# Kernel tuning notes

Hardware: AMD Instinct MI355X
Metric: run time of the kernel (lower is better)

The kernel has to match this reference:

```python
import jax, jax.numpy as jnp
import numpy as np

T, B, D, O = 2048, 32, 512, 512


def setup_inputs() -> dict:
    key = jax.random.key(0)
    ks = jax.random.split(key, 12)
    s = 0.02
    return {
        "word": jax.random.normal(ks[0], (T, B, D), dtype=jnp.float32),
        "Wf": jax.random.normal(ks[1], (D, D), dtype=jnp.float32) * s,
        "bf": jax.random.normal(ks[2], (D,), dtype=jnp.float32) * s,
        "Wi": jax.random.normal(ks[3], (D, D), dtype=jnp.float32) * s,
        "bi": jax.random.normal(ks[4], (D,), dtype=jnp.float32) * s,
        "Wz": jax.random.normal(ks[5], (D, D), dtype=jnp.float32) * s,
        "bz": jax.random.normal(ks[6], (D,), dtype=jnp.float32) * s,
        "Wo": jax.random.normal(ks[7], (D, D), dtype=jnp.float32) * s,
        "bo": jax.random.normal(ks[8], (D,), dtype=jnp.float32) * s,
        "Wy": jax.random.normal(ks[9], (O, D), dtype=jnp.float32) * s,
        "by": jax.random.normal(ks[10], (O,), dtype=jnp.float32) * s,
    }


def reference(word, Wf, bf, Wi, bi, Wz, bz, Wo, bo, Wy, by):
    # Faithful to the original buggy module:
    #  - forward discards the updated cell state, so c == 0 every step and
    #    the zf gate (wf) never affects the output.
    #  - z and zo reuse wi(hidden) instead of wz/wo(hidden).
    #  - the same Linear is applied to letter and hidden, so bias is doubled
    #    in zi (and zf).
    Bsz, Dd = word.shape[1], word.shape[2]

    def step(h, x):  # h: [B, D], x: [B, D]
        hWi = h @ Wi.T                                  # reused by zi, z, zo
        zi = jax.nn.sigmoid(x @ Wi.T + hWi + 2.0 * bi)
        z = jax.nn.sigmoid(x @ Wz.T + bz + hWi + bi)
        zo = jax.nn.sigmoid(x @ Wo.T + bo + hWi + bi)
        c = zi * z                                      # zf * 0 + zi * z
        h_new = zo * jnp.tanh(c)
        return h_new, None

    h0 = jnp.zeros((Bsz, Dd), dtype=word.dtype)
    h_final, _ = jax.lax.scan(step, h0, word)
    # original computes wy(hidden) every step but only returns the last one
    output = h_final @ Wy.T + by                        # [B, O]
    return output
```

## Files before the change

kernel.cpp:

```cpp
#include <hip/hip_runtime.h>

typedef unsigned int u32;
typedef unsigned short u16;
typedef _Float16 f16;
typedef f16 f16x2 __attribute__((ext_vector_type(2)));

__device__ __forceinline__ float fdot2(u32 a, u32 b, float c) {
#if __has_builtin(__builtin_amdgcn_fdot2)
    return __builtin_amdgcn_fdot2(__builtin_bit_cast(f16x2, a),
                                  __builtin_bit_cast(f16x2, b), c, false);
#else
    f16x2 av = __builtin_bit_cast(f16x2, a), bv = __builtin_bit_cast(f16x2, b);
    c += (float)av[0] * (float)bv[0];
    c += (float)av[1] * (float)bv[1];
    return c;
#endif
}

__device__ __forceinline__ u32 pack2h(float a, float b) {
    f16x2 h; h[0] = (f16)a; h[1] = (f16)b;
    return __builtin_bit_cast(u32, h);
}
__device__ __forceinline__ float h2f(u16 x) { return (float)__builtin_bit_cast(f16, x); }
__device__ __forceinline__ u16 f2h(float x) { f16 h = (f16)x; return __builtin_bit_cast(u16, h); }

__device__ __forceinline__ float fexp(float x) {
#if __has_builtin(__builtin_amdgcn_exp2f)
    return __builtin_amdgcn_exp2f(x * 1.44269504088896f);
#else
    return __expf(x);
#endif
}
__device__ __forceinline__ float frcp(float x) {
#if __has_builtin(__builtin_amdgcn_rcpf)
    return __builtin_amdgcn_rcpf(x);
#else
    return 1.0f / x;
#endif
}
__device__ __forceinline__ float fsigmoid(float x) { return frcp(1.0f + fexp(-x)); }
__device__ __forceinline__ float ftanh_pos(float x) { return 1.0f - 2.0f * frcp(fexp(2.0f * x) + 1.0f); }

template <int CTRL>
__device__ __forceinline__ float dpp_xor_add(float x) {
    int y = __builtin_amdgcn_update_dpp(0, __builtin_bit_cast(int, x), CTRL, 0xF, 0xF, true);
    return x + __builtin_bit_cast(float, y);
}

__global__ __launch_bounds__(256) void k0_pack(const float* __restrict__ Wi,
                                               const float* __restrict__ Wy,
                                               u32* __restrict__ WpkT,
                                               u32* __restrict__ Wypk) {
    const int bx = blockIdx.x, tid = threadIdx.x;
    if (bx < 512) {
        const float2 v = *(const float2*)(Wi + (size_t)bx * 512 + 2 * tid);
        WpkT[(size_t)bx * 256 + tid] = pack2h(v.x, v.y);
    } else {
        const int p = bx - 512;
        #pragma unroll
        for (int r = 0; r < 2; ++r) {
            const int d = tid + 256 * r;
            Wypk[(size_t)p * 512 + d] =
                pack2h(Wy[(size_t)d * 512 + 2 * p], Wy[(size_t)d * 512 + 2 * p + 1]);
        }
    }
}

__global__ __launch_bounds__(256) void k1_gates(
    const float* __restrict__ word,
    const float* __restrict__ Wi, const float* __restrict__ Wz, const float* __restrict__ Wo,
    const float* __restrict__ bi, const float* __restrict__ bz, const float* __restrict__ bo,
    u16* __restrict__ Xi, u16* __restrict__ Xz, u16* __restrict__ Xo)
{
    __shared__ u32 ws2[3][16][132];
    __shared__ u32 xs2[2][16][36];

    const int tid = threadIdx.x;
    const int d_l = tid & 63;
    const int bq  = tid >> 6;
    const int t0  = blockIdx.x * 2;
    const int d0  = blockIdx.y * 128;

    const float* Wg[3] = {Wi, Wz, Wo};

    float acc[2][2][8][3];
    #pragma unroll
    for (int tt = 0; tt < 2; ++tt)
        #pragma unroll
        for (int db = 0; db < 2; ++db)
            #pragma unroll
            for (int j = 0; j < 8; ++j)
                #pragma unroll
                for (int g = 0; g < 3; ++g) acc[tt][db][j][g] = 0.0f;

    for (int k0 = 0; k0 < 512; k0 += 32) {
        {
            const int p = tid & 15, bg = tid >> 4;
            #pragma unroll
            for (int tt = 0; tt < 2; ++tt)
                #pragma unroll
                for (int j = 0; j < 2; ++j) {
                    const int bb = bg * 2 + j;
                    const float2 v = *(const float2*)(word + (((size_t)(t0 + tt) * 32 + bb) * 512 + k0 + 2 * p));
                    xs2[tt][p][bb] = pack2h(v.x, v.y);
                }
        }
        {
            const int q = tid & 7, r = tid >> 3;
            #pragma unroll
            for (int g = 0; g < 3; ++g)
                #pragma unroll
                for (int s = 0; s < 4; ++s) {
                    const int i = r + 32 * s;
                    const float4 v = *(const float4*)(Wg[g] + ((size_t)(d0 + i) * 512 + k0 + 4 * q));
                    ws2[g][2 * q + 0][i] = pack2h(v.x, v.y);
                    ws2[g][2 * q + 1][i] = pack2h(v.z, v.w);
                }
        }
        __syncthreads();
        #pragma unroll 2
        for (int p = 0; p < 16; ++p) {
            u32 x2[2][8];
            #pragma unroll
            for (int tt = 0; tt < 2; ++tt) {
                const uint4* xr = (const uint4*)&xs2[tt][p][bq * 8];
                uint4 xa = xr[0], xb = xr[1];
                x2[tt][0] = xa.x; x2[tt][1] = xa.y; x2[tt][2] = xa.z; x2[tt][3] = xa.w;
                x2[tt][4] = xb.x; x2[tt][5] = xb.y; x2[tt][6] = xb.z; x2[tt][7] = xb.w;
            }
            u32 w2[3][2];
            #pragma unroll
            for (int g = 0; g < 3; ++g) {
                w2[g][0] = ws2[g][p][d_l];
                w2[g][1] = ws2[g][p][d_l + 64];
            }
            #pragma unroll
            for (int tt = 0; tt < 2; ++tt)
                #pragma unroll
                for (int db = 0; db < 2; ++db)
                    #pragma unroll
                    for (int j = 0; j < 8; ++j)
                        #pragma unroll
                        for (int g = 0; g < 3; ++g)
                            acc[tt][db][j][g] = fdot2(x2[tt][j], w2[g][db], acc[tt][db][j][g]);
        }
        __syncthreads();
    }

    #pragma unroll
    for (int db = 0; db < 2; ++db) {
        const int d = d0 + 64 * db + d_l;
        const float b0 = 2.0f * bi[d];
        const float b1 = bz[d] + bi[d];
        const float b2 = bo[d] + bi[d];
        #pragma unroll
        for (int tt = 0; tt < 2; ++tt)
            #pragma unroll
            for (int j = 0; j < 8; ++j) {
                const size_t o = ((size_t)(t0 + tt) * 32 + (bq * 8 + j)) * 512 + d;
                Xi[o] = f2h(acc[tt][db][j][0] + b0);
                Xz[o] = f2h(acc[tt][db][j][1] + b1);
                Xo[o] = f2h(acc[tt][db][j][2] + b2);
            }
    }
}

__global__ __launch_bounds__(512, 2) void k2_recur(
    const u16* __restrict__ Xi, const u16* __restrict__ Xz, const u16* __restrict__ Xo,
    const u32* __restrict__ WpkT, const u32* __restrict__ Wypk,
    const float* __restrict__ by, float* __restrict__ out)
{
    __shared__ alignas(16) u32 wlds[7][2048];
    __shared__ alignas(16) u16 hbuf[2][512];

    const int b = blockIdx.x;
    const int tid = threadIdx.x;
    const int kq = tid & 3, dg = tid >> 2;

    u32 w[4][57];
    #pragma unroll
    for (int j = 0; j < 4; ++j) {
        const u32* row = WpkT + (size_t)(4 * dg + j) * 256 + 64 * kq;
        const uint4* rv = (const uint4*)row;
        #pragma unroll
        for (int i = 0; i < 14; ++i) {
            uint4 v = rv[i];
            w[j][4 * i + 0] = v.x; w[j][4 * i + 1] = v.y;
            w[j][4 * i + 2] = v.z; w[j][4 * i + 3] = v.w;
        }
        uint4 t14 = rv[14], t15 = rv[15];
        w[j][56] = t14.x;
        wlds[0][tid * 4 + j] = t14.y;
        wlds[1][tid * 4 + j] = t14.z;
        wlds[2][tid * 4 + j] = t14.w;
        wlds[3][tid * 4 + j] = t15.x;
        wlds[4][tid * 4 + j] = t15.y;
        wlds[5][tid * 4 + j] = t15.z;
        wlds[6][tid * 4 + j] = t15.w;
    }
    hbuf[0][tid] = (u16)0;
    __syncthreads();

    const uint4* hq0 = (const uint4*)&hbuf[0][0] + 16 * kq;
    const uint4* hq1 = (const uint4*)&hbuf[1][0] + 16 * kq;
    const uint4* wldv = (const uint4*)&wlds[0][0];

    size_t idx0 = (size_t)b * 512 + tid;
    u16 xi_c = Xi[idx0], xz_c = Xz[idx0], xo_c = Xo[idx0];

    for (int t = 0; t < 2048; ++t) {
        const int cur = t & 1, nxt = cur ^ 1;
        const int tn = (t + 1) & 2047;
        const size_t idxn = ((size_t)tn * 32 + b) * 512 + tid;
        u16 xi_n = Xi[idxn], xz_n = Xz[idxn], xo_n = Xo[idxn];

        const uint4* hv = cur ? hq1 : hq0;
        float a0 = 0.f, a1 = 0.f, a2 = 0.f, a3 = 0.f;
        #pragma unroll
        for (int i = 0; i < 14; ++i) {
            uint4 hc = hv[i];
            a0 = fdot2(hc.x, w[0][4 * i + 0], a0);
            a1 = fdot2(hc.x, w[1][4 * i + 0], a1);
            a2 = fdot2(hc.x, w[2][4 * i + 0], a2);
            a3 = fdot2(hc.x, w[3][4 * i + 0], a3);
            a0 = fdot2(hc.y, w[0][4 * i + 1], a0);
            a1 = fdot2(hc.y, w[1][4 * i + 1], a1);
            a2 = fdot2(hc.y, w[2][4 * i + 1], a2);
            a3 = fdot2(hc.y, w[3][4 * i + 1], a3);
            a0 = fdot2(hc.z, w[0][4 * i + 2], a0);
            a1 = fdot2(hc.z, w[1][4 * i + 2], a1);
            a2 = fdot2(hc.z, w[2][4 * i + 2], a2);
            a3 = fdot2(hc.z, w[3][4 * i + 2], a3);
            a0 = fdot2(hc.w, w[0][4 * i + 3], a0);
            a1 = fdot2(hc.w, w[1][4 * i + 3], a1);
            a2 = fdot2(hc.w, w[2][4 * i + 3], a2);
            a3 = fdot2(hc.w, w[3][4 * i + 3], a3);
        }
        {
            uint4 h14 = hv[14], h15 = hv[15];
            uint4 wl0 = wldv[0 * 512 + tid];
            uint4 wl1 = wldv[1 * 512 + tid];
            uint4 wl2 = wldv[2 * 512 + tid];
            uint4 wl3 = wldv[3 * 512 + tid];
            uint4 wl4 = wldv[4 * 512 + tid];
            uint4 wl5 = wldv[5 * 512 + tid];
            uint4 wl6 = wldv[6 * 512 + tid];
            a0 = fdot2(h14.x, w[0][56], a0);
            a1 = fdot2(h14.x, w[1][56], a1);
            a2 = fdot2(h14.x, w[2][56], a2);
            a3 = fdot2(h14.x, w[3][56], a3);
            a0 = fdot2(h14.y, wl0.x, a0); a1 = fdot2(h14.y, wl0.y, a1);
            a2 = fdot2(h14.y, wl0.z, a2); a3 = fdot2(h14.y, wl0.w, a3);
            a0 = fdot2(h14.z, wl1.x, a0); a1 = fdot2(h14.z, wl1.y, a1);
            a2 = fdot2(h14.z, wl1.z, a2); a3 = fdot2(h14.z, wl1.w, a3);
            a0 = fdot2(h14.w, wl2.x, a0); a1 = fdot2(h14.w, wl2.y, a1);
            a2 = fdot2(h14.w, wl2.z, a2); a3 = fdot2(h14.w, wl2.w, a3);
            a0 = fdot2(h15.x, wl3.x, a0); a1 = fdot2(h15.x, wl3.y, a1);
            a2 = fdot2(h15.x, wl3.z, a2); a3 = fdot2(h15.x, wl3.w, a3);
            a0 = fdot2(h15.y, wl4.x, a0); a1 = fdot2(h15.y, wl4.y, a1);
            a2 = fdot2(h15.y, wl4.z, a2); a3 = fdot2(h15.y, wl4.w, a3);
            a0 = fdot2(h15.z, wl5.x, a0); a1 = fdot2(h15.z, wl5.y, a1);
            a2 = fdot2(h15.z, wl5.z, a2); a3 = fdot2(h15.z, wl5.w, a3);
            a0 = fdot2(h15.w, wl6.x, a0); a1 = fdot2(h15.w, wl6.y, a1);
            a2 = fdot2(h15.w, wl6.z, a2); a3 = fdot2(h15.w, wl6.w, a3);
        }
        a0 = dpp_xor_add<0xB1>(a0); a1 = dpp_xor_add<0xB1>(a1);
        a2 = dpp_xor_add<0xB1>(a2); a3 = dpp_xor_add<0xB1>(a3);
        a0 = dpp_xor_add<0x4E>(a0); a1 = dpp_xor_add<0x4E>(a1);
        a2 = dpp_xor_add<0x4E>(a2); a3 = dpp_xor_add<0x4E>(a3);
        float v = a0;
        v = (kq == 1) ? a1 : v;
        v = (kq == 2) ? a2 : v;
        v = (kq == 3) ? a3 : v;

        const float zi = fsigmoid(h2f(xi_c) + v);
        const float z  = fsigmoid(h2f(xz_c) + v);
        const float zo = fsigmoid(h2f(xo_c) + v);
        const float hn = zo * ftanh_pos(zi * z);

        hbuf[nxt][tid] = f2h(hn);
        __syncthreads();

        xi_c = xi_n; xz_c = xz_n; xo_c = xo_n;
    }

    {
        const uint4* hv = (const uint4*)&hbuf[0][0];
        float a0 = 0.f, a1 = 0.f, a2 = 0.f, a3 = 0.f;
        #pragma unroll
        for (int i = 0; i < 64; ++i) {
            uint4 hc = hv[i];
            a0 = fdot2(hc.x, Wypk[(size_t)(4 * i + 0) * 512 + tid], a0);
            a1 = fdot2(hc.y, Wypk[(size_t)(4 * i + 1) * 512 + tid], a1);
            a2 = fdot2(hc.z, Wypk[(size_t)(4 * i + 2) * 512 + tid], a2);
            a3 = fdot2(hc.w, Wypk[(size_t)(4 * i + 3) * 512 + tid], a3);
        }
        out[(size_t)b * 512 + tid] = (a0 + a1) + (a2 + a3) + by[tid];
    }
}

extern "C" void kernel_launch(void* const* d_in, const int* in_sizes, int n_in,
                              void* d_out, int out_size, void* d_ws, size_t ws_size,
                              hipStream_t stream) {
    const float* word = (const float*)d_in[0];
    const float* Wi = (const float*)d_in[3];
    const float* bi = (const float*)d_in[4];
    const float* Wz = (const float*)d_in[5];
    const float* bz = (const float*)d_in[6];
    const float* Wo = (const float*)d_in[7];
    const float* bo = (const float*)d_in[8];
    const float* Wy = (const float*)d_in[9];
    const float* by = (const float*)d_in[10];
    float* out = (float*)d_out;

    char* ws = (char*)d_ws;
    const size_t XN = (size_t)2048 * 32 * 512 * sizeof(u16);
    u16* Xi = (u16*)(ws);
    u16* Xz = (u16*)(ws + XN);
    u16* Xo = (u16*)(ws + 2 * XN);
    u32* WpkT = (u32*)(ws + 3 * XN);
    u32* Wypk = (u32*)(ws + 3 * XN + (size_t)524288);

    k0_pack<<<768, 256, 0, stream>>>(Wi, Wy, WpkT, Wypk);

    dim3 g1(1024, 4);
    k1_gates<<<g1, 256, 0, stream>>>(word, Wi, Wz, Wo, bi, bz, bo, Xi, Xz, Xo);

    k2_recur<<<32, 512, 0, stream>>>(Xi, Xz, Xo, WpkT, Wypk, by, out);
}
```

Before: 4.811 ms.

## Halve recurrent block to 256 threads with 8 outputs per thread

The recurrent kernel now runs 256 threads per batch row instead of 512. Each thread computes two hidden outputs across eight weight rows, keeping 13 uint4 per row in registers, part of the rest in LDS, and re-reading the last chunk from global memory every step. The hidden-state buffer is padded into four 288-byte segments to avoid LDS bank conflicts, and gate inputs are loaded as f16 pairs. The aim is to cut per-step barrier cost and wave count on the serial critical path. In exchange it adds register pressure and global weight loads inside the time loop.

```diff
diff --git a/kernel.cpp b/kernel.cpp
--- a/kernel.cpp
+++ b/kernel.cpp
@@ -165,137 +165,239 @@
     }
 }
 
-__global__ __launch_bounds__(512, 2) void k2_recur(
+__global__ __launch_bounds__(256, 1) void k2_recur(
     const u16* __restrict__ Xi, const u16* __restrict__ Xz, const u16* __restrict__ Xo,
     const u32* __restrict__ WpkT, const u32* __restrict__ Wypk,
     const float* __restrict__ by, float* __restrict__ out)
 {
-    __shared__ alignas(16) u32 wlds[7][2048];
-    __shared__ alignas(16) u16 hbuf[2][512];
-
-    const int b = blockIdx.x;
+    __shared__ alignas(16) uint4 wldsv[15 * 256];
+    __shared__ alignas(16) u16 hbuf[2][4 * 144];
+
+    const int b   = blockIdx.x;
     const int tid = threadIdx.x;
-    const int kq = tid & 3, dg = tid >> 2;
-
-    u32 w[4][57];
+    const int kq  = tid & 3;
+    const int dg  = tid >> 2;
+
+    const uint4* WpkT4 = (const uint4*)WpkT;
+
+    uint4 wv[8][13];
     #pragma unroll
-    for (int j = 0; j < 4; ++j) {
-        const u32* row = WpkT + (size_t)(4 * dg + j) * 256 + 64 * kq;
-        const uint4* rv = (const uint4*)row;
-        #pragma unroll
-        for (int i = 0; i < 14; ++i) {
-            uint4 v = rv[i];
-            w[j][4 * i + 0] = v.x; w[j][4 * i + 1] = v.y;
-            w[j][4 * i + 2] = v.z; w[j][4 * i + 3] = v.w;
-        }
-        uint4 t14 = rv[14], t15 = rv[15];
-        w[j][56] = t14.x;
-        wlds[0][tid * 4 + j] = t14.y;
-        wlds[1][tid * 4 + j] = t14.z;
-        wlds[2][tid * 4 + j] = t14.w;
-        wlds[3][tid * 4 + j] = t15.x;
-        wlds[4][tid * 4 + j] = t15.y;
-        wlds[5][tid * 4 + j] = t15.z;
-        wlds[6][tid * 4 + j] = t15.w;
-    }
-    hbuf[0][tid] = (u16)0;
+    for (int j = 0; j < 8; ++j) {
+        const uint4* rv = WpkT4 + (size_t)(8 * dg + j) * 64 + 16 * kq;
+        #pragma unroll
+        for (int i = 0; i < 13; ++i) wv[j][i] = rv[i];
+        if (j < 7) {
+            wldsv[(2 * j + 0) * 256 + tid] = rv[13];
+            wldsv[(2 * j + 1) * 256 + tid] = rv[14];
+        } else {
+            wldsv[14 * 256 + tid] = rv[13];
+        }
+    }
+
+    const int d0 = 8 * dg + 2 * kq;
+    const int hq_ = d0 >> 7, hj_ = d0 & 127;
+    u32* hw0 = (u32*)((char*)&hbuf[0][0] + hq_ * 288 + 2 * hj_);
+    u32* hw1 = (u32*)((char*)&hbuf[1][0] + hq_ * 288 + 2 * hj_);
+    *hw0 = 0u;
     __syncthreads();
 
-    const uint4* hq0 = (const uint4*)&hbuf[0][0] + 16 * kq;
-    const uint4* hq1 = (const uint4*)&hbuf[1][0] + 16 * kq;
-    const uint4* wldv = (const uint4*)&wlds[0][0];
-
-    size_t idx0 = (size_t)b * 512 + tid;
-    u16 xi_c = Xi[idx0], xz_c = Xz[idx0], xo_c = Xo[idx0];
+    const uint4* hv0 = (const uint4*)((const char*)&hbuf[0][0] + kq * 288);
+    const uint4* hv1 = (const uint4*)((const char*)&hbuf[1][0] + kq * 288);
+
+    u32 xi_c = *(const u32*)(Xi + (size_t)b * 512 + d0);
+    u32 xz_c = *(const u32*)(Xz + (size_t)b * 512 + d0);
+    u32 xo_c = *(const u32*)(Xo + (size_t)b * 512 + d0);
 
     for (int t = 0; t < 2048; ++t) {
-        const int cur = t & 1, nxt = cur ^ 1;
+        const int cur = t & 1;
         const int tn = (t + 1) & 2047;
-        const size_t idxn = ((size_t)tn * 32 + b) * 512 + tid;
-        u16 xi_n = Xi[idxn], xz_n = Xz[idxn], xo_n = Xo[idxn];
-
-        const uint4* hv = cur ? hq1 : hq0;
+        const size_t xbase = ((size_t)tn * 32 + b) * 512 + d0;
+        const u32 xi_n = *(const u32*)(Xi + xbase);
+        const u32 xz_n = *(const u32*)(Xz + xbase);
+        const u32 xo_n = *(const u32*)(Xo + xbase);
+
+        const uint4* hv = cur ? hv1 : hv0;
         float a0 = 0.f, a1 = 0.f, a2 = 0.f, a3 = 0.f;
-        #pragma unroll
-        for (int i = 0; i < 14; ++i) {
+        float a4 = 0.f, a5 = 0.f, a6 = 0.f, a7 = 0.f;
+
+        #pragma unroll
+        for (int i = 0; i < 8; ++i) {
             uint4 hc = hv[i];
-            a0 = fdot2(hc.x, w[0][4 * i + 0], a0);
-            a1 = fdot2(hc.x, w[1][4 * i + 0], a1);
-            a2 = fdot2(hc.x, w[2][4 * i + 0], a2);
-            a3 = fdot2(hc.x, w[3][4 * i + 0], a3);
-            a0 = fdot2(hc.y, w[0][4 * i + 1], a0);
-            a1 = fdot2(hc.y, w[1][4 * i + 1], a1);
-            a2 = fdot2(hc.y, w[2][4 * i + 1], a2);
-            a3 = fdot2(hc.y, w[3][4 * i + 1], a3);
-            a0 = fdot2(hc.z, w[0][4 * i + 2], a0);
-            a1 = fdot2(hc.z, w[1][4 * i + 2], a1);
-            a2 = fdot2(hc.z, w[2][4 * i + 2], a2);
-            a3 = fdot2(hc.z, w[3][4 * i + 2], a3);
-            a0 = fdot2(hc.w, w[0][4 * i + 3], a0);
-            a1 = fdot2(hc.w, w[1][4 * i + 3], a1);
-            a2 = fdot2(hc.w, w[2][4 * i + 3], a2);
-            a3 = fdot2(hc.w, w[3][4 * i + 3], a3);
-        }
+            a0 = fdot2(hc.x, wv[0][i].x, a0); a0 = fdot2(hc.y, wv[0][i].y, a0);
+            a0 = fdot2(hc.z, wv[0][i].z, a0); a0 = fdot2(hc.w, wv[0][i].w, a0);
+            a1 = fdot2(hc.x, wv[1][i].x, a1); a1 = fdot2(hc.y, wv[1][i].y, a1);
+            a1 = fdot2(hc.z, wv[1][i].z, a1); a1 = fdot2(hc.w, wv[1][i].w, a1);
+            a2 = fdot2(hc.x, wv[2][i].x, a2); a2 = fdot2(hc.y, wv[2][i].y, a2);
+            a2 = fdot2(hc.z, wv[2][i].z, a2); a2 = fdot2(hc.w, wv[2][i].w, a2);
+            a3 = fdot2(hc.x, wv[3][i].x, a3); a3 = fdot2(hc.y, wv[3][i].y, a3);
+            a3 = fdot2(hc.z, wv[3][i].z, a3); a3 = fdot2(hc.w, wv[3][i].w, a3);
+            a4 = fdot2(hc.x, wv[4][i].x, a4); a4 = fdot2(hc.y, wv[4][i].y, a4);
+            a4 = fdot2(hc.z, wv[4][i].z, a4); a4 = fdot2(hc.w, wv[4][i].w, a4);
+            a5 = fdot2(hc.x, wv[5][i].x, a5); a5 = fdot2(hc.y, wv[5][i].y, a5);
+            a5 = fdot2(hc.z, wv[5][i].z, a5); a5 = fdot2(hc.w, wv[5][i].w, a5);
+            a6 = fdot2(hc.x, wv[6][i].x, a6); a6 = fdot2(hc.y, wv[6][i].y, a6);
+            a6 = fdot2(hc.z, wv[6][i].z, a6); a6 = fdot2(hc.w, wv[6][i].w, a6);
+            a7 = fdot2(hc.x, wv[7][i].x, a7); a7 = fdot2(hc.y, wv[7][i].y, a7);
+            a7 = fdot2(hc.z, wv[7][i].z, a7); a7 = fdot2(hc.w, wv[7][i].w, a7);
+        }
+
+        uint4 g0 = WpkT4[(size_t)(8 * dg + 0) * 64 + 16 * kq + 15];
+        uint4 g1 = WpkT4[(size_t)(8 * dg + 1) * 64 + 16 * kq + 15];
+        uint4 g2 = WpkT4[(size_t)(8 * dg + 2) * 64 + 16 * kq + 15];
+        uint4 g3 = WpkT4[(size_t)(8 * dg + 3) * 64 + 16 * kq + 15];
+        uint4 g4 = WpkT4[(size_t)(8 * dg + 4) * 64 + 16 * kq + 15];
+        uint4 g5 = WpkT4[(size_t)(8 * dg + 5) * 64 + 16 * kq + 15];
+        uint4 g6 = WpkT4[(size_t)(8 * dg + 6) * 64 + 16 * kq + 15];
+        uint4 g7a = WpkT4[(size_t)(8 * dg + 7) * 64 + 16 * kq + 14];
+        uint4 g7b = WpkT4[(size_t)(8 * dg + 7) * 64 + 16 * kq + 15];
+
+        #pragma unroll
+        for (int i = 8; i < 13; ++i) {
+            uint4 hc = hv[i];
+            a0 = fdot2(hc.x, wv[0][i].x, a0); a0 = fdot2(hc.y, wv[0][i].y, a0);
+            a0 = fdot2(hc.z, wv[0][i].z, a0); a0 = fdot2(hc.w, wv[0][i].w, a0);
+            a1 = fdot2(hc.x, wv[1][i].x, a1); a1 = fdot2(hc.y, wv[1][i].y, a1);
+            a1 = fdot2(hc.z, wv[1][i].z, a1); a1 = fdot2(hc.w, wv[1][i].w, a1);
+            a2 = fdot2(hc.x, wv[2][i].x, a2); a2 = fdot2(hc.y, wv[2][i].y, a2);
+            a2 = fdot2(hc.z, wv[2][i].z, a2); a2 = fdot2(hc.w, wv[2][i].w, a2);
+            a3 = fdot2(hc.x, wv[3][i].x, a3); a3 = fdot2(hc.y, wv[3][i].y, a3);
+            a3 = fdot2(hc.z, wv[3][i].z, a3); a3 = fdot2(hc.w, wv[3][i].w, a3);
+            a4 = fdot2(hc.x, wv[4][i].x, a4); a4 = fdot2(hc.y, wv[4][i].y, a4);
+            a4 = fdot2(hc.z, wv[4][i].z, a4); a4 = fdot2(hc.w, wv[4][i].w, a4);
+            a5 = fdot2(hc.x, wv[5][i].x, a5); a5 = fdot2(hc.y, wv[5][i].y, a5);
+            a5 = fdot2(hc.z, wv[5][i].z, a5); a5 = fdot2(hc.w, wv[5][i].w, a5);
+            a6 = fdot2(hc.x, wv[6][i].x, a6); a6 = fdot2(hc.y, wv[6][i].y, a6);
+            a6 = fdot2(hc.z, wv[6][i].z, a6); a6 = fdot2(hc.w, wv[6][i].w, a6);
+            a7 = fdot2(hc.x, wv[7][i].x, a7); a7 = fdot2(hc.y, wv[7][i].y, a7);
+            a7 = fdot2(hc.z, wv[7][i].z, a7); a7 = fdot2(hc.w, wv[7][i].w, a7);
+        }
+
         {
-            uint4 h14 = hv[14], h15 = hv[15];
-            uint4 wl0 = wldv[0 * 512 + tid];
-            uint4 wl1 = wldv[1 * 512 + tid];
-            uint4 wl2 = wldv[2 * 512 + tid];
-            uint4 wl3 = wldv[3 * 512 + tid];
-            uint4 wl4 = wldv[4 * 512 + tid];
-            uint4 wl5 = wldv[5 * 512 + tid];
-            uint4 wl6 = wldv[6 * 512 + tid];
-            a0 = fdot2(h14.x, w[0][56], a0);
-            a1 = fdot2(h14.x, w[1][56], a1);
-            a2 = fdot2(h14.x, w[2][56], a2);
-            a3 = fdot2(h14.x, w[3][56], a3);
-            a0 = fdot2(h14.y, wl0.x, a0); a1 = fdot2(h14.y, wl0.y, a1);
-            a2 = fdot2(h14.y, wl0.z, a2); a3 = fdot2(h14.y, wl0.w, a3);
-            a0 = fdot2(h14.z, wl1.x, a0); a1 = fdot2(h14.z, wl1.y, a1);
-            a2 = fdot2(h14.z, wl1.z, a2); a3 = fdot2(h14.z, wl1.w, a3);
-            a0 = fdot2(h14.w, wl2.x, a0); a1 = fdot2(h14.w, wl2.y, a1);
-            a2 = fdot2(h14.w, wl2.z, a2); a3 = fdot2(h14.w, wl2.w, a3);
-            a0 = fdot2(h15.x, wl3.x, a0); a1 = fdot2(h15.x, wl3.y, a1);
-            a2 = fdot2(h15.x, wl3.z, a2); a3 = fdot2(h15.x, wl3.w, a3);
-            a0 = fdot2(h15.y, wl4.x, a0); a1 = fdot2(h15.y, wl4.y, a1);
-            a2 = fdot2(h15.y, wl4.z, a2); a3 = fdot2(h15.y, wl4.w, a3);
-            a0 = fdot2(h15.z, wl5.x, a0); a1 = fdot2(h15.z, wl5.y, a1);
-            a2 = fdot2(h15.z, wl5.z, a2); a3 = fdot2(h15.z, wl5.w, a3);
-            a0 = fdot2(h15.w, wl6.x, a0); a1 = fdot2(h15.w, wl6.y, a1);
-            a2 = fdot2(h15.w, wl6.z, a2); a3 = fdot2(h15.w, wl6.w, a3);
-        }
+            uint4 hc = hv[13];
+            uint4 l0 = wldsv[0 * 256 + tid];
+            uint4 l1 = wldsv[2 * 256 + tid];
+            uint4 l2 = wldsv[4 * 256 + tid];
+            uint4 l3 = wldsv[6 * 256 + tid];
+            uint4 l4 = wldsv[8 * 256 + tid];
+            uint4 l5 = wldsv[10 * 256 + tid];
+            uint4 l6 = wldsv[12 * 256 + tid];
+            uint4 l7 = wldsv[14 * 256 + tid];
+            a0 = fdot2(hc.x, l0.x, a0); a0 = fdot2(hc.y, l0.y, a0);
+            a0 = fdot2(hc.z, l0.z, a0); a0 = fdot2(hc.w, l0.w, a0);
+            a1 = fdot2(hc.x, l1.x, a1); a1 = fdot2(hc.y, l1.y, a1);
+            a1 = fdot2(hc.z, l1.z, a1); a1 = fdot2(hc.w, l1.w, a1);
+            a2 = fdot2(hc.x, l2.x, a2); a2 = fdot2(hc.y, l2.y, a2);
+            a2 = fdot2(hc.z, l2.z, a2); a2 = fdot2(hc.w, l2.w, a2);
+            a3 = fdot2(hc.x, l3.x, a3); a3 = fdot2(hc.y, l3.y, a3);
+            a3 = fdot2(hc.z, l3.z, a3); a3 = fdot2(hc.w, l3.w, a3);
+            a4 = fdot2(hc.x, l4.x, a4); a4 = fdot2(hc.y, l4.y, a4);
+            a4 = fdot2(hc.z, l4.z, a4); a4 = fdot2(hc.w, l4.w, a4);
+            a5 = fdot2(hc.x, l5.x, a5); a5 = fdot2(hc.y, l5.y, a5);
+            a5 = fdot2(hc.z, l5.z, a5); a5 = fdot2(hc.w, l5.w, a5);
+            a6 = fdot2(hc.x, l6.x, a6); a6 = fdot2(hc.y, l6.y, a6);
+            a6 = fdot2(hc.z, l6.z, a6); a6 = fdot2(hc.w, l6.w, a6);
+            a7 = fdot2(hc.x, l7.x, a7); a7 = fdot2(hc.y, l7.y, a7);
+            a7 = fdot2(hc.z, l7.z, a7); a7 = fdot2(hc.w, l7.w, a7);
+        }
+        {
+            uint4 hc = hv[14];
+            uint4 l0 = wldsv[1 * 256 + tid];
+            uint4 l1 = wldsv[3 * 256 + tid];
+            uint4 l2 = wldsv[5 * 256 + tid];
+            uint4 l3 = wldsv[7 * 256 + tid];
+            uint4 l4 = wldsv[9 * 256 + tid];
+            uint4 l5 = wldsv[11 * 256 + tid];
+            uint4 l6 = wldsv[13 * 256 + tid];
+            a0 = fdot2(hc.x, l0.x, a0); a0 = fdot2(hc.y, l0.y, a0);
+            a0 = fdot2(hc.z, l0.z, a0); a0 = fdot2(hc.w, l0.w, a0);
+            a1 = fdot2(hc.x, l1.x, a1); a1 = fdot2(hc.y, l1.y, a1);
+            a1 = fdot2(hc.z, l1.z, a1); a1 = fdot2(hc.w, l1.w, a1);
+            a2 = fdot2(hc.x, l2.x, a2); a2 = fdot2(hc.y, l2.y, a2);
+            a2 = fdot2(hc.z, l2.z, a2); a2 = fdot2(hc.w, l2.w, a2);
+            a3 = fdot2(hc.x, l3.x, a3); a3 = fdot2(hc.y, l3.y, a3);
+            a3 = fdot2(hc.z, l3.z, a3); a3 = fdot2(hc.w, l3.w, a3);
+            a4 = fdot2(hc.x, l4.x, a4); a4 = fdot2(hc.y, l4.y, a4);
+            a4 = fdot2(hc.z, l4.z, a4); a4 = fdot2(hc.w, l4.w, a4);
+            a5 = fdot2(hc.x, l5.x, a5); a5 = fdot2(hc.y, l5.y, a5);
+            a5 = fdot2(hc.z, l5.z, a5); a5 = fdot2(hc.w, l5.w, a5);
+            a6 = fdot2(hc.x, l6.x, a6); a6 = fdot2(hc.y, l6.y, a6);
+            a6 = fdot2(hc.z, l6.z, a6); a6 = fdot2(hc.w, l6.w, a6);
+            a7 = fdot2(hc.x, g7a.x, a7); a7 = fdot2(hc.y, g7a.y, a7);
+            a7 = fdot2(hc.z, g7a.z, a7); a7 = fdot2(hc.w, g7a.w, a7);
+        }
+        {
+            uint4 hc = hv[15];
+            a0 = fdot2(hc.x, g0.x, a0); a0 = fdot2(hc.y, g0.y, a0);
+            a0 = fdot2(hc.z, g0.z, a0); a0 = fdot2(hc.w, g0.w, a0);
+            a1 = fdot2(hc.x, g1.x, a1); a1 = fdot2(hc.y, g1.y, a1);
+            a1 = fdot2(hc.z, g1.z, a1); a1 = fdot2(hc.w, g1.w, a1);
+            a2 = fdot2(hc.x, g2.x, a2); a2 = fdot2(hc.y, g2.y, a2);
+            a2 = fdot2(hc.z, g2.z, a2); a2 = fdot2(hc.w, g2.w, a2);
+            a3 = fdot2(hc.x, g3.x, a3); a3 = fdot2(hc.y, g3.y, a3);
+            a3 = fdot2(hc.z, g3.z, a3); a3 = fdot2(hc.w, g3.w, a3);
+            a4 = fdot2(hc.x, g4.x, a4); a4 = fdot2(hc.y, g4.y, a4);
+            a4 = fdot2(hc.z, g4.z, a4); a4 = fdot2(hc.w, g4.w, a4);
+            a5 = fdot2(hc.x, g5.x, a5); a5 = fdot2(hc.y, g5.y, a5);
+            a5 = fdot2(hc.z, g5.z, a5); a5 = fdot2(hc.w, g5.w, a5);
+            a6 = fdot2(hc.x, g6.x, a6); a6 = fdot2(hc.y, g6.y, a6);
+            a6 = fdot2(hc.z, g6.z, a6); a6 = fdot2(hc.w, g6.w, a6);
+            a7 = fdot2(hc.x, g7b.x, a7); a7 = fdot2(hc.y, g7b.y, a7);
+            a7 = fdot2(hc.z, g7b.z, a7); a7 = fdot2(hc.w, g7b.w, a7);
+        }
+
         a0 = dpp_xor_add<0xB1>(a0); a1 = dpp_xor_add<0xB1>(a1);
         a2 = dpp_xor_add<0xB1>(a2); a3 = dpp_xor_add<0xB1>(a3);
+        a4 = dpp_xor_add<0xB1>(a4); a5 = dpp_xor_add<0xB1>(a5);
+        a6 = dpp_xor_add<0xB1>(a6); a7 = dpp_xor_add<0xB1>(a7);
         a0 = dpp_xor_add<0x4E>(a0); a1 = dpp_xor_add<0x4E>(a1);
         a2 = dpp_xor_add<0x4E>(a2); a3 = dpp_xor_add<0x4E>(a3);
-        float v = a0;
-        v = (kq == 1) ? a1 : v;
-        v = (kq == 2) ? a2 : v;
-        v = (kq == 3) ? a3 : v;
-
-        const float zi = fsigmoid(h2f(xi_c) + v);
-        const float z  = fsigmoid(h2f(xz_c) + v);
-        const float zo = fsigmoid(h2f(xo_c) + v);
-        const float hn = zo * ftanh_pos(zi * z);
-
-        hbuf[nxt][tid] = f2h(hn);
+        a4 = dpp_xor_add<0x4E>(a4); a5 = dpp_xor_add<0x4E>(a5);
+        a6 = dpp_xor_add<0x4E>(a6); a7 = dpp_xor_add<0x4E>(a7);
+
+        const float v0 = (kq & 2) ? ((kq & 1) ? a6 : a4) : ((kq & 1) ? a2 : a0);
+        const float v1 = (kq & 2) ? ((kq & 1) ? a7 : a5) : ((kq & 1) ? a3 : a1);
+
+        const f16x2 xi2 = __builtin_bit_cast(f16x2, xi_c);
+        const f16x2 xz2 = __builtin_bit_cast(f16x2, xz_c);
+        const f16x2 xo2 = __builtin_bit_cast(f16x2, xo_c);
+
+        const float zi0 = fsigmoid((float)xi2[0] + v0);
+        const float z0  = fsigmoid((float)xz2[0] + v0);
+        const float zo0 = fsigmoid((float)xo2[0] + v0);
+        const float hn0 = zo0 * ftanh_pos(zi0 * z0);
+        const float zi1 = fsigmoid((float)xi2[1] + v1);
+        const float z1  = fsigmoid((float)xz2[1] + v1);
+        const float zo1 = fsigmoid((float)xo2[1] + v1);
+        const float hn1 = zo1 * ftanh_pos(zi1 * z1);
+
+        const u32 hwv = (u32)f2h(hn0) | ((u32)f2h(hn1) << 16);
+        *(cur ? hw0 : hw1) = hwv;
         __syncthreads();
 
         xi_c = xi_n; xz_c = xz_n; xo_c = xo_n;
     }
 
     {
-        const uint4* hv = (const uint4*)&hbuf[0][0];
-        float a0 = 0.f, a1 = 0.f, a2 = 0.f, a3 = 0.f;
-        #pragma unroll
-        for (int i = 0; i < 64; ++i) {
-            uint4 hc = hv[i];
-            a0 = fdot2(hc.x, Wypk[(size_t)(4 * i + 0) * 512 + tid], a0);
-            a1 = fdot2(hc.y, Wypk[(size_t)(4 * i + 1) * 512 + tid], a1);
-            a2 = fdot2(hc.z, Wypk[(size_t)(4 * i + 2) * 512 + tid], a2);
-            a3 = fdot2(hc.w, Wypk[(size_t)(4 * i + 3) * 512 + tid], a3);
-        }
-        out[(size_t)b * 512 + tid] = (a0 + a1) + (a2 + a3) + by[tid];
+        float e0 = 0.f, e1 = 0.f;
+        #pragma unroll
+        for (int q = 0; q < 4; ++q) {
+            const uint4* hq = (const uint4*)((const char*)&hbuf[0][0] + q * 288);
+            #pragma unroll
+            for (int i = 0; i < 16; ++i) {
+                uint4 hc = hq[i];
+                const int p = 64 * q + 4 * i;
+                e0 = fdot2(hc.x, Wypk[(size_t)(p + 0) * 512 + tid], e0);
+                e0 = fdot2(hc.y, Wypk[(size_t)(p + 1) * 512 + tid], e0);
+                e0 = fdot2(hc.z, Wypk[(size_t)(p + 2) * 512 + tid], e0);
+                e0 = fdot2(hc.w, Wypk[(size_t)(p + 3) * 512 + tid], e0);
+                e1 = fdot2(hc.x, Wypk[(size_t)(p + 0) * 512 + tid + 256], e1);
+                e1 = fdot2(hc.y, Wypk[(size_t)(p + 1) * 512 + tid + 256], e1);
+                e1 = fdot2(hc.z, Wypk[(size_t)(p + 2) * 512 + tid + 256], e1);
+                e1 = fdot2(hc.w, Wypk[(size_t)(p + 3) * 512 + tid + 256], e1);
+            }
+        }
+        out[(size_t)b * 512 + tid]       = e0 + by[tid];
+        out[(size_t)b * 512 + tid + 256] = e1 + by[tid + 256];
     }
 }
 
@@ -326,5 +428,5 @@
     dim3 g1(1024, 4);
     k1_gates<<<g1, 256, 0, stream>>>(word, Wi, Wz, Wo, bi, bz, bo, Xi, Xz, Xo);
 
-    k2_recur<<<32, 512, 0, stream>>>(Xi, Xz, Xo, WpkT, Wypk, by, out);
-}
+    k2_recur<<<32, 256, 0, stream>>>(Xi, Xz, Xo, WpkT, Wypk, by, out);
+}
```

After: 6.214 ms. +29.2%, slower.
